# Optimization experiments

Measured on AMD Instinct MI355X. Metric: run time of the kernel, lower is better.

The kernel has to match this reference:

```python
import jax, jax.numpy as jnp
import numpy as np

B, T, S, D, F = 4, 2048, 2048, 256, 1024
EPS = 1e-5


def setup_inputs() -> dict:
    key = jax.random.key(0)
    ks = jax.random.split(key, 24)
    def lin(kw, kb, din, dout):
        w = jax.random.normal(kw, (din, dout), jnp.float32) / np.sqrt(din)
        b = jax.random.normal(kb, (dout,), jnp.float32) * 0.01
        return w, b
    Wq1, bq1 = lin(ks[0], ks[1], D, D)
    Wk1, bk1 = lin(ks[2], ks[3], D, D)
    Wv1, bv1 = lin(ks[4], ks[5], D, D)
    Wq2, bq2 = lin(ks[6], ks[7], D, D)
    Wk2, bk2 = lin(ks[8], ks[9], D, D)
    Wv2, bv2 = lin(ks[10], ks[11], D, D)
    W1, b1 = lin(ks[12], ks[13], D, F)
    W2, b2 = lin(ks[14], ks[15], F, D)
    y = jax.random.normal(ks[16], (B, T, D), jnp.float32)
    Z = jax.random.normal(ks[17], (B, S, D), jnp.float32)
    target_mask = jnp.tril(jnp.ones((T, T), jnp.int32))  # causal 0/1 mask
    return dict(y=y, Z=Z, target_mask=target_mask,
                Wq1=Wq1, bq1=bq1, Wk1=Wk1, bk1=bk1, Wv1=Wv1, bv1=bv1,
                Wq2=Wq2, bq2=bq2, Wk2=Wk2, bk2=bk2, Wv2=Wv2, bv2=bv2,
                W1=W1, b1=b1, W2=W2, b2=b2,
                g1=jnp.ones((D,), jnp.float32), be1=jnp.zeros((D,), jnp.float32),
                g2=jnp.ones((D,), jnp.float32), be2=jnp.zeros((D,), jnp.float32),
                g3=jnp.ones((D,), jnp.float32), be3=jnp.zeros((D,), jnp.float32))


def _ln(x, g, b):
    m = x.mean(-1, keepdims=True)
    v = ((x - m) ** 2).mean(-1, keepdims=True)
    return (x - m) / jnp.sqrt(v + EPS) * g + b


def _attn(Q, K, V, mask=None):
    scale = 1.0 / np.sqrt(Q.shape[-1]).astype(np.float32)
    scores = jnp.einsum('btd,bsd->bts', Q, K) * scale  # [B,T,S]
    if mask is not None:
        scores = jnp.where(mask == 0, -jnp.inf, scores)
    probs = jax.nn.softmax(scores, axis=-1)
    return jnp.einsum('bts,bsd->btd', probs, V)


def reference(y, Z, target_mask, Wq1, bq1, Wk1, bk1, Wv1, bv1,
              Wq2, bq2, Wk2, bk2, Wv2, bv2, W1, b1, W2, b2,
              g1, be1, g2, be2, g3, be3):
    # self attention
    sa = _attn(y @ Wq1 + bq1, y @ Wk1 + bk1, y @ Wv1 + bv1, target_mask)
    y1 = _ln(y + sa, g1, be1)
    # cross attention
    ca = _attn(y1 @ Wq2 + bq2, Z @ Wk2 + bk2, Z @ Wv2 + bv2)
    y2 = _ln(y1 + ca, g2, be2)
    # FFN
    ffn = jax.nn.relu(y2 @ W1 + b1) @ W2 + b2
    return _ln(y2 + ffn, g3, be3)
```

## Files before the change

kernel.cpp:

```cpp
#include <hip/hip_runtime.h>

#define B_ 4
#define T_ 2048
#define S_ 2048
#define D_ 256
#define F_ 1024

typedef unsigned short ushort_t;
typedef __bf16 v8bf __attribute__((ext_vector_type(8)));
typedef float v4f __attribute__((ext_vector_type(4)));
typedef __attribute__((address_space(1))) const unsigned int gas_uint;
typedef __attribute__((address_space(3))) unsigned int las_uint;

__device__ __forceinline__ ushort_t f2bf(float f) {
  unsigned u = __float_as_uint(f);
  unsigned r = (u + 0x7FFFu + ((u >> 16) & 1u)) >> 16;
  return (ushort_t)r;
}

struct WP { const float* s; ushort_t* d; int K, N; };
struct WP8 { WP m[8]; };

__global__ void prep_weights_k(WP8 a) {
  WP w = a.m[blockIdx.z];
  int k0 = blockIdx.x * 64, n0 = blockIdx.y * 64;
  if (k0 >= w.K || n0 >= w.N) return;
  __shared__ ushort_t tile[64][65];
  int tx = threadIdx.x, ty = threadIdx.y;
  for (int r = ty; r < 64; r += 4)
    tile[r][tx] = f2bf(w.s[(size_t)(k0 + r) * w.N + n0 + tx]);
  __syncthreads();
  for (int r = ty; r < 64; r += 4)
    w.d[(size_t)(n0 + r) * w.K + k0 + tx] = tile[tx][r];
}

__global__ void cvt_k(const float* __restrict__ a, ushort_t* __restrict__ oa,
                      const float* __restrict__ b, ushort_t* __restrict__ ob) {
  int i = blockIdx.x * 256 + threadIdx.x;
  const float* s = blockIdx.y ? b : a;
  ushort_t* d = blockIdx.y ? ob : oa;
  size_t off = (size_t)i * 8;
  float4 v0 = *(const float4*)(s + off);
  float4 v1 = *(const float4*)(s + off + 4);
  union { ushort_t u[8]; uint4 v; } pk;
  pk.u[0] = f2bf(v0.x); pk.u[1] = f2bf(v0.y); pk.u[2] = f2bf(v0.z); pk.u[3] = f2bf(v0.w);
  pk.u[4] = f2bf(v1.x); pk.u[5] = f2bf(v1.y); pk.u[6] = f2bf(v1.z); pk.u[7] = f2bf(v1.w);
  *(uint4*)(d + off) = pk.v;
}

__global__ void transpose_bf16_k(const ushort_t* __restrict__ in, ushort_t* __restrict__ out,
                                 int rows, int cols) {
  in  += (size_t)blockIdx.z * rows * cols;
  out += (size_t)blockIdx.z * rows * cols;
  __shared__ ushort_t tile[64][65];
  int r0 = blockIdx.x * 64, c0 = blockIdx.y * 64;
  int tx = threadIdx.x, ty = threadIdx.y;
  for (int r = ty; r < 64; r += 4)
    tile[r][tx] = in[(size_t)(r0 + r) * cols + c0 + tx];
  __syncthreads();
  for (int r = ty; r < 64; r += 4)
    out[(size_t)(c0 + r) * rows + r0 + tx] = tile[tx][r];
}

template<bool RELU>
__global__ __launch_bounds__(256, 2) void gemm_bt(
    const ushort_t* __restrict__ A, int lda, long long sAz,
    const ushort_t* __restrict__ Bt, int ldb, long long sBz,
    const float* __restrict__ bias,
    float* __restrict__ Cf, ushort_t* __restrict__ Cb, int ldc, long long sCz,
    int K, float alpha, int causal, int crow0) {
  const int n0 = blockIdx.x * 64, m0 = blockIdx.y * 128;
  if (causal && n0 > crow0 + m0 + 127) return;
  A  += (long long)blockIdx.z * sAz;
  Bt += (long long)blockIdx.z * sBz;
  const long long coff = (long long)blockIdx.z * sCz;
  const int t = threadIdx.x, lane = t & 63, wv = t >> 6;
  const int wm = wv >> 1, wn = wv & 1;
  const int kslot = lane >> 4, l15 = lane & 15;
  __shared__ __align__(16) char smem[24576];
  char* sA = smem;
  char* sB = smem + 16384;

  v4f acc[4][2];
  v4f zero = {0.f, 0.f, 0.f, 0.f};
#pragma unroll
  for (int m = 0; m < 4; ++m)
#pragma unroll
    for (int n = 0; n < 2; ++n) acc[m][n] = zero;

  for (int kk = 0; kk < K; kk += 64) {
    __syncthreads();
#pragma unroll
    for (int q = 0; q < 4; ++q) {
      int g = q * 256 + t;
      int row = g >> 3, j = g & 7;
      const ushort_t* src = A + (long long)(m0 + row) * lda + kk + ((j ^ (row & 7)) << 3);
      __builtin_amdgcn_global_load_lds((gas_uint*)src,
          (las_uint*)(sA + q * 4096 + (wv << 10)), 16, 0, 0);
    }
#pragma unroll
    for (int q = 0; q < 2; ++q) {
      int g = q * 256 + t;
      int row = g >> 3, j = g & 7;
      const ushort_t* src = Bt + (long long)(n0 + row) * ldb + kk + ((j ^ (row & 7)) << 3);
      __builtin_amdgcn_global_load_lds((gas_uint*)src,
          (las_uint*)(sB + q * 4096 + (wv << 10)), 16, 0, 0);
    }
    __syncthreads();
#pragma unroll
    for (int ks = 0; ks < 2; ++ks) {
      v8bf af[4]; v8bf bfr[2];
#pragma unroll
      for (int m = 0; m < 4; ++m) {
        int row = wm * 64 + m * 16 + l15;
        int gs = (ks * 4 + kslot) ^ (row & 7);
        af[m] = *(const v8bf*)(sA + ((row * 8 + gs) << 4));
      }
#pragma unroll
      for (int n = 0; n < 2; ++n) {
        int row = wn * 32 + n * 16 + l15;
        int gs = (ks * 4 + kslot) ^ (row & 7);
        bfr[n] = *(const v8bf*)(sB + ((row * 8 + gs) << 4));
      }
#pragma unroll
      for (int m = 0; m < 4; ++m)
#pragma unroll
        for (int n = 0; n < 2; ++n)
          acc[m][n] = __builtin_amdgcn_mfma_f32_16x16x32_bf16(af[m], bfr[n], acc[m][n], 0, 0, 0);
    }
  }
#pragma unroll
  for (int m = 0; m < 4; ++m) {
    int grow0 = m0 + wm * 64 + m * 16 + (kslot << 2);
#pragma unroll
    for (int n = 0; n < 2; ++n) {
      int gcol = n0 + wn * 32 + n * 16 + l15;
      float bb = bias ? bias[gcol] : 0.f;
#pragma unroll
      for (int i = 0; i < 4; ++i) {
        float v = acc[m][n][i] * alpha + bb;
        if (RELU) v = fmaxf(v, 0.f);
        long long off = coff + (long long)(grow0 + i) * ldc + gcol;
        if (Cf) Cf[off] = v;
        if (Cb) Cb[off] = f2bf(v);
      }
    }
  }
}

__global__ __launch_bounds__(256) void softmax_k(float* scores, int causal, int crow0) {
  int row = blockIdx.x;
  float* rp = scores + ((size_t)blockIdx.y * T_ + row) * S_;
  int t = threadIdx.x;
  int valid = causal ? crow0 + row + 1 : S_;
  float x[8];
  float4 v0 = *(const float4*)(rp + t * 8);
  float4 v1 = *(const float4*)(rp + t * 8 + 4);
  x[0] = v0.x; x[1] = v0.y; x[2] = v0.z; x[3] = v0.w;
  x[4] = v1.x; x[5] = v1.y; x[6] = v1.z; x[7] = v1.w;
  float m = -3.0e38f;
#pragma unroll
  for (int j = 0; j < 8; ++j) if (t * 8 + j < valid) m = fmaxf(m, x[j]);
  for (int mk = 1; mk < 64; mk <<= 1) m = fmaxf(m, __shfl_xor(m, mk));
  __shared__ float rbuf[8];
  if ((t & 63) == 0) rbuf[t >> 6] = m;
  __syncthreads();
  m = fmaxf(fmaxf(rbuf[0], rbuf[1]), fmaxf(rbuf[2], rbuf[3]));
  float p[8]; float l = 0.f;
#pragma unroll
  for (int j = 0; j < 8; ++j) { p[j] = (t * 8 + j < valid) ? __expf(x[j] - m) : 0.f; l += p[j]; }
  for (int mk = 1; mk < 64; mk <<= 1) l += __shfl_xor(l, mk);
  if ((t & 63) == 0) rbuf[4 + (t >> 6)] = l;
  __syncthreads();
  l = rbuf[4] + rbuf[5] + rbuf[6] + rbuf[7];
  float inv = 1.f / l;
  union { ushort_t u[8]; uint4 v; } pk;
#pragma unroll
  for (int j = 0; j < 8; ++j) pk.u[j] = f2bf(p[j] * inv);
  __syncthreads();
  *(uint4*)((ushort_t*)rp + t * 8) = pk.v;
}

__global__ __launch_bounds__(256) void add_ln_k(
    const float* __restrict__ base, const float* __restrict__ delta,
    const float* __restrict__ g, const float* __restrict__ be,
    float* __restrict__ outf, ushort_t* __restrict__ outb) {
  int row = blockIdx.x * 4 + (threadIdx.x >> 6);
  int lane = threadIdx.x & 63;
  size_t off = (size_t)row * 256 + lane * 4;
  float4 xv = *(const float4*)(base + off);
  float4 dv = *(const float4*)(delta + off);
  float s0 = xv.x + dv.x, s1 = xv.y + dv.y, s2 = xv.z + dv.z, s3 = xv.w + dv.w;
  float sum = s0 + s1 + s2 + s3;
  for (int mk = 1; mk < 64; mk <<= 1) sum += __shfl_xor(sum, mk);
  float mean = sum * (1.f / 256.f);
  float e0 = s0 - mean, e1 = s1 - mean, e2 = s2 - mean, e3 = s3 - mean;
  float ss = e0 * e0 + e1 * e1 + e2 * e2 + e3 * e3;
  for (int mk = 1; mk < 64; mk <<= 1) ss += __shfl_xor(ss, mk);
  float rstd = rsqrtf(ss * (1.f / 256.f) + 1e-5f);
  float4 gv = *(const float4*)(g + lane * 4);
  float4 bv = *(const float4*)(be + lane * 4);
  float o0 = e0 * rstd * gv.x + bv.x, o1 = e1 * rstd * gv.y + bv.y;
  float o2 = e2 * rstd * gv.z + bv.z, o3 = e3 * rstd * gv.w + bv.w;
  float4 ov; ov.x = o0; ov.y = o1; ov.z = o2; ov.w = o3;
  *(float4*)(outf + off) = ov;
  if (outb) {
    union { ushort_t u[4]; uint2 v; } pk;
    pk.u[0] = f2bf(o0); pk.u[1] = f2bf(o1); pk.u[2] = f2bf(o2); pk.u[3] = f2bf(o3);
    *(uint2*)(outb + off) = pk.v;
  }
}

extern "C" void kernel_launch(void* const* d_in, const int* in_sizes, int n_in,
                              void* d_out, int out_size, void* d_ws, size_t ws_size,
                              hipStream_t stream) {
  const float* y   = (const float*)d_in[0];
  const float* Z   = (const float*)d_in[1];
  const float* Wq1 = (const float*)d_in[3];  const float* bq1 = (const float*)d_in[4];
  const float* Wk1 = (const float*)d_in[5];  const float* bk1 = (const float*)d_in[6];
  const float* Wv1 = (const float*)d_in[7];  const float* bv1 = (const float*)d_in[8];
  const float* Wq2 = (const float*)d_in[9];  const float* bq2 = (const float*)d_in[10];
  const float* Wk2 = (const float*)d_in[11]; const float* bk2 = (const float*)d_in[12];
  const float* Wv2 = (const float*)d_in[13]; const float* bv2 = (const float*)d_in[14];
  const float* W1  = (const float*)d_in[15]; const float* b1  = (const float*)d_in[16];
  const float* W2  = (const float*)d_in[17]; const float* b2  = (const float*)d_in[18];
  const float* g1  = (const float*)d_in[19]; const float* be1 = (const float*)d_in[20];
  const float* g2  = (const float*)d_in[21]; const float* be2 = (const float*)d_in[22];
  const float* g3  = (const float*)d_in[23]; const float* be3 = (const float*)d_in[24];
  float* out = (float*)d_out;

  char* p = (char*)d_ws;
  auto alloc = [&](size_t sz) { char* r = p; p += (sz + 255) & ~(size_t)255; return r; };
  const size_t NBT = (size_t)B_ * T_ * D_;
  ushort_t* Wq1t = (ushort_t*)alloc(D_ * D_ * 2);
  ushort_t* Wk1t = (ushort_t*)alloc(D_ * D_ * 2);
  ushort_t* Wv1t = (ushort_t*)alloc(D_ * D_ * 2);
  ushort_t* Wq2t = (ushort_t*)alloc(D_ * D_ * 2);
  ushort_t* Wk2t = (ushort_t*)alloc(D_ * D_ * 2);
  ushort_t* Wv2t = (ushort_t*)alloc(D_ * D_ * 2);
  ushort_t* W1t  = (ushort_t*)alloc((size_t)F_ * D_ * 2);
  ushort_t* W2t  = (ushort_t*)alloc((size_t)D_ * F_ * 2);
  ushort_t* yb  = (ushort_t*)alloc(NBT * 2);
  ushort_t* Zb  = (ushort_t*)alloc(NBT * 2);
  float*    y1f = (float*)alloc(NBT * 4);
  ushort_t* y1b = (ushort_t*)alloc(NBT * 2);
  float*    y2f = (float*)alloc(NBT * 4);
  ushort_t* y2b = (ushort_t*)alloc(NBT * 2);
  ushort_t* Qb = (ushort_t*)alloc(NBT * 2);
  ushort_t* Kb = (ushort_t*)alloc(NBT * 2);
  ushort_t* Vb = (ushort_t*)alloc(NBT * 2);
  ushort_t* Vt = (ushort_t*)alloc(NBT * 2);
  ushort_t* Hb = Qb;
  float* tmp = (float*)alloc(NBT * 4);
  float* scores = (float*)p;
  size_t remain = (ws_size > (size_t)(p - (char*)d_ws))
                      ? ws_size - (size_t)(p - (char*)d_ws) : 0;
  const size_t rowb = (size_t)S_ * 4;
  int CH = 0, TC = 0;
  if (remain >= (size_t)B_ * T_ * rowb)      { CH = B_; TC = T_; }
  else if (remain >= (size_t)T_ * rowb)      { CH = 1;  TC = T_; }
  else {
    int tc = (int)(remain / (rowb * 128)) * 128;
    if (tc > T_) tc = T_;
    CH = 1; TC = tc;
  }

  WP8 wp;
  wp.m[0] = {Wq1, Wq1t, D_, D_}; wp.m[1] = {Wk1, Wk1t, D_, D_};
  wp.m[2] = {Wv1, Wv1t, D_, D_}; wp.m[3] = {Wq2, Wq2t, D_, D_};
  wp.m[4] = {Wk2, Wk2t, D_, D_}; wp.m[5] = {Wv2, Wv2t, D_, D_};
  wp.m[6] = {W1, W1t, D_, F_};   wp.m[7] = {W2, W2t, F_, D_};
  prep_weights_k<<<dim3(16, 16, 8), dim3(64, 4), 0, stream>>>(wp);
  cvt_k<<<dim3((int)(NBT / 8 / 256), 2), 256, 0, stream>>>(y, yb, Z, Zb);

  auto gemm = [&](const ushort_t* A, int lda, long long sAz,
                  const ushort_t* Bt, int ldb, long long sBz,
                  const float* bias, float* Cf, ushort_t* Cb, int ldc, long long sCz,
                  int M, int N, int K, float alpha, int causal, bool relu, int Zn, int crow0) {
    dim3 g(N / 64, M / 128, Zn);
    if (relu)
      gemm_bt<true><<<g, 256, 0, stream>>>(A, lda, sAz, Bt, ldb, sBz, bias, Cf, Cb, ldc, sCz, K, alpha, causal, crow0);
    else
      gemm_bt<false><<<g, 256, 0, stream>>>(A, lda, sAz, Bt, ldb, sBz, bias, Cf, Cb, ldc, sCz, K, alpha, causal, crow0);
  };

  auto attention = [&](const ushort_t* Q, const ushort_t* Kc, const ushort_t* Vc,
                       float* attout, int causal) {
    transpose_bf16_k<<<dim3(S_ / 64, D_ / 64, B_), dim3(64, 4), 0, stream>>>(Vc, Vt, S_, D_);
    if (TC <= 0) return;
    for (int b0 = 0; b0 < B_; b0 += CH) {
      for (int t0 = 0; t0 < T_; t0 += TC) {
        int rows = (t0 + TC <= T_) ? TC : (T_ - t0);
        gemm(Q + ((size_t)b0 * T_ + t0) * D_, D_, (long long)T_ * D_,
             Kc + (size_t)b0 * S_ * D_, D_, (long long)S_ * D_,
             nullptr, scores, nullptr, S_, (long long)T_ * S_,
             rows, S_, D_, 0.0625f, causal, false, CH, t0);
        softmax_k<<<dim3(rows, CH), 256, 0, stream>>>(scores, causal, t0);
        gemm((const ushort_t*)scores, 2 * S_, (long long)T_ * 2 * S_,
             Vt + (size_t)b0 * D_ * S_, S_, (long long)D_ * S_,
             nullptr, attout + ((size_t)b0 * T_ + t0) * D_, nullptr, D_, (long long)T_ * D_,
             rows, D_, S_, 1.f, 0, false, CH, 0);
      }
    }
  };

  gemm(yb, D_, 0, Wq1t, D_, 0, bq1, nullptr, Qb, D_, 0, B_ * T_, D_, D_, 1.f, 0, false, 1, 0);
  gemm(yb, D_, 0, Wk1t, D_, 0, bk1, nullptr, Kb, D_, 0, B_ * T_, D_, D_, 1.f, 0, false, 1, 0);
  gemm(yb, D_, 0, Wv1t, D_, 0, bv1, nullptr, Vb, D_, 0, B_ * T_, D_, D_, 1.f, 0, false, 1, 0);
  attention(Qb, Kb, Vb, tmp, 1);
  add_ln_k<<<dim3(B_ * T_ / 4), 256, 0, stream>>>(y, tmp, g1, be1, y1f, y1b);

  gemm(y1b, D_, 0, Wq2t, D_, 0, bq2, nullptr, Qb, D_, 0, B_ * T_, D_, D_, 1.f, 0, false, 1, 0);
  gemm(Zb,  D_, 0, Wk2t, D_, 0, bk2, nullptr, Kb, D_, 0, B_ * S_, D_, D_, 1.f, 0, false, 1, 0);
  gemm(Zb,  D_, 0, Wv2t, D_, 0, bv2, nullptr, Vb, D_, 0, B_ * S_, D_, D_, 1.f, 0, false, 1, 0);
  attention(Qb, Kb, Vb, tmp, 0);
  add_ln_k<<<dim3(B_ * T_ / 4), 256, 0, stream>>>(y1f, tmp, g2, be2, y2f, y2b);

  gemm(y2b, D_, 0, W1t, D_, 0, b1, nullptr, Hb, F_, 0, B_ * T_, F_, D_, 1.f, 0, true, 1, 0);
  gemm(Hb, F_, 0, W2t, F_, 0, b2, tmp, nullptr, D_, 0, B_ * T_, D_, F_, 1.f, 0, false, 1, 0);
  add_ln_k<<<dim3(B_ * T_ / 4), 256, 0, stream>>>(y2f, tmp, g3, be3, out, nullptr);
}
```

Baseline: 364.5 us.

## Fuse QKV projections, store scores in bf16, and skip masked K-tiles in PV

Merges the Q/K/V projection GEMMs into one wide GEMM writing an interleaved QKV buffer with packed biases, and merges the cross-attention K/V projections the same way. Attention scores are now written directly as bf16 instead of fp32, so softmax and the probability-by-value GEMM move half the bytes. The probability-by-value GEMM also stops its K loop at the causal diagonal. This relies on the transposed weight buffers being laid out contiguously so one GEMM covers Wq/Wk/Wv, and pre-softmax scores lose precision when rounded to bf16.

```diff
diff --git a/kernel.cpp b/kernel.cpp
--- a/kernel.cpp
+++ b/kernel.cpp
@@ -16,6 +16,9 @@
   unsigned u = __float_as_uint(f);
   unsigned r = (u + 0x7FFFu + ((u >> 16) & 1u)) >> 16;
   return (ushort_t)r;
+}
+__device__ __forceinline__ float bf2f(ushort_t u) {
+  return __uint_as_float((unsigned)u << 16);
 }
 
 struct WP { const float* s; ushort_t* d; int K, N; };
@@ -32,6 +35,14 @@
   __syncthreads();
   for (int r = ty; r < 64; r += 4)
     w.d[(size_t)(n0 + r) * w.K + k0 + tx] = tile[tx][r];
+}
+
+__global__ void pack_bias_k(const float* bq1, const float* bk1, const float* bv1,
+                            const float* bk2, const float* bv2,
+                            float* bqkv1, float* bkv2) {
+  int t = blockIdx.x * 256 + threadIdx.x;
+  if (t < 768) bqkv1[t] = (t < 256) ? bq1[t] : (t < 512) ? bk1[t - 256] : bv1[t - 512];
+  if (t < 512) bkv2[t] = (t < 256) ? bk2[t] : bv2[t - 256];
 }
 
 __global__ void cvt_k(const float* __restrict__ a, ushort_t* __restrict__ oa,
@@ -48,15 +59,16 @@
   *(uint4*)(d + off) = pk.v;
 }
 
-__global__ void transpose_bf16_k(const ushort_t* __restrict__ in, ushort_t* __restrict__ out,
+__global__ void transpose_bf16_k(const ushort_t* __restrict__ in, long long sIz, int ldin,
+                                 ushort_t* __restrict__ out, long long sOz,
                                  int rows, int cols) {
-  in  += (size_t)blockIdx.z * rows * cols;
-  out += (size_t)blockIdx.z * rows * cols;
+  in  += (size_t)blockIdx.z * sIz;
+  out += (size_t)blockIdx.z * sOz;
   __shared__ ushort_t tile[64][65];
   int r0 = blockIdx.x * 64, c0 = blockIdx.y * 64;
   int tx = threadIdx.x, ty = threadIdx.y;
   for (int r = ty; r < 64; r += 4)
-    tile[r][tx] = in[(size_t)(r0 + r) * cols + c0 + tx];
+    tile[r][tx] = in[(size_t)(r0 + r) * ldin + c0 + tx];
   __syncthreads();
   for (int r = ty; r < 64; r += 4)
     out[(size_t)(c0 + r) * rows + r0 + tx] = tile[tx][r];
@@ -68,9 +80,10 @@
     const ushort_t* __restrict__ Bt, int ldb, long long sBz,
     const float* __restrict__ bias,
     float* __restrict__ Cf, ushort_t* __restrict__ Cb, int ldc, long long sCz,
-    int K, float alpha, int causal, int crow0) {
+    int K, float alpha, int causal, int kcausal, int crow0) {
   const int n0 = blockIdx.x * 64, m0 = blockIdx.y * 128;
   if (causal && n0 > crow0 + m0 + 127) return;
+  const int Keff = kcausal ? ((crow0 + m0 + 128 < K) ? crow0 + m0 + 128 : K) : K;
   A  += (long long)blockIdx.z * sAz;
   Bt += (long long)blockIdx.z * sBz;
   const long long coff = (long long)blockIdx.z * sCz;
@@ -88,7 +101,7 @@
 #pragma unroll
     for (int n = 0; n < 2; ++n) acc[m][n] = zero;
 
-  for (int kk = 0; kk < K; kk += 64) {
+  for (int kk = 0; kk < Keff; kk += 64) {
     __syncthreads();
 #pragma unroll
     for (int q = 0; q < 4; ++q) {
@@ -148,16 +161,16 @@
   }
 }
 
-__global__ __launch_bounds__(256) void softmax_k(float* scores, int causal, int crow0) {
+__global__ __launch_bounds__(256) void softmax_k(ushort_t* sc, int causal, int crow0) {
   int row = blockIdx.x;
-  float* rp = scores + ((size_t)blockIdx.y * T_ + row) * S_;
+  ushort_t* rp = sc + ((size_t)blockIdx.y * T_ + row) * S_;
   int t = threadIdx.x;
   int valid = causal ? crow0 + row + 1 : S_;
+  union { ushort_t u[8]; uint4 v; } in;
+  in.v = *(const uint4*)(rp + t * 8);
   float x[8];
-  float4 v0 = *(const float4*)(rp + t * 8);
-  float4 v1 = *(const float4*)(rp + t * 8 + 4);
-  x[0] = v0.x; x[1] = v0.y; x[2] = v0.z; x[3] = v0.w;
-  x[4] = v1.x; x[5] = v1.y; x[6] = v1.z; x[7] = v1.w;
+#pragma unroll
+  for (int j = 0; j < 8; ++j) x[j] = bf2f(in.u[j]);
   float m = -3.0e38f;
 #pragma unroll
   for (int j = 0; j < 8; ++j) if (t * 8 + j < valid) m = fmaxf(m, x[j]);
@@ -177,8 +190,7 @@
   union { ushort_t u[8]; uint4 v; } pk;
 #pragma unroll
   for (int j = 0; j < 8; ++j) pk.u[j] = f2bf(p[j] * inv);
-  __syncthreads();
-  *(uint4*)((ushort_t*)rp + t * 8) = pk.v;
+  *(uint4*)(rp + t * 8) = pk.v;
 }
 
 __global__ __launch_bounds__(256) void add_ln_k(
@@ -240,22 +252,22 @@
   ushort_t* Wv2t = (ushort_t*)alloc(D_ * D_ * 2);
   ushort_t* W1t  = (ushort_t*)alloc((size_t)F_ * D_ * 2);
   ushort_t* W2t  = (ushort_t*)alloc((size_t)D_ * F_ * 2);
+  float* bqkv1 = (float*)alloc(768 * 4);
+  float* bkv2  = (float*)alloc(512 * 4);
   ushort_t* yb  = (ushort_t*)alloc(NBT * 2);
   ushort_t* Zb  = (ushort_t*)alloc(NBT * 2);
   float*    y1f = (float*)alloc(NBT * 4);
   ushort_t* y1b = (ushort_t*)alloc(NBT * 2);
   float*    y2f = (float*)alloc(NBT * 4);
   ushort_t* y2b = (ushort_t*)alloc(NBT * 2);
-  ushort_t* Qb = (ushort_t*)alloc(NBT * 2);
-  ushort_t* Kb = (ushort_t*)alloc(NBT * 2);
-  ushort_t* Vb = (ushort_t*)alloc(NBT * 2);
-  ushort_t* Vt = (ushort_t*)alloc(NBT * 2);
-  ushort_t* Hb = Qb;
+  ushort_t* QKVb = (ushort_t*)alloc((size_t)B_ * T_ * 768 * 2);
+  ushort_t* Vt   = (ushort_t*)alloc(NBT * 2);
+  ushort_t* Hb = QKVb;
   float* tmp = (float*)alloc(NBT * 4);
-  float* scores = (float*)p;
+  ushort_t* sc = (ushort_t*)p;
   size_t remain = (ws_size > (size_t)(p - (char*)d_ws))
                       ? ws_size - (size_t)(p - (char*)d_ws) : 0;
-  const size_t rowb = (size_t)S_ * 4;
+  const size_t rowb = (size_t)S_ * 2;
   int CH = 0, TC = 0;
   if (remain >= (size_t)B_ * T_ * rowb)      { CH = B_; TC = T_; }
   else if (remain >= (size_t)T_ * rowb)      { CH = 1;  TC = T_; }
@@ -271,52 +283,58 @@
   wp.m[4] = {Wk2, Wk2t, D_, D_}; wp.m[5] = {Wv2, Wv2t, D_, D_};
   wp.m[6] = {W1, W1t, D_, F_};   wp.m[7] = {W2, W2t, F_, D_};
   prep_weights_k<<<dim3(16, 16, 8), dim3(64, 4), 0, stream>>>(wp);
+  pack_bias_k<<<dim3(5), 256, 0, stream>>>(bq1, bk1, bv1, bk2, bv2, bqkv1, bkv2);
   cvt_k<<<dim3((int)(NBT / 8 / 256), 2), 256, 0, stream>>>(y, yb, Z, Zb);
 
   auto gemm = [&](const ushort_t* A, int lda, long long sAz,
                   const ushort_t* Bt, int ldb, long long sBz,
                   const float* bias, float* Cf, ushort_t* Cb, int ldc, long long sCz,
-                  int M, int N, int K, float alpha, int causal, bool relu, int Zn, int crow0) {
+                  int M, int N, int K, float alpha, int causal, int kcausal,
+                  bool relu, int Zn, int crow0) {
     dim3 g(N / 64, M / 128, Zn);
     if (relu)
-      gemm_bt<true><<<g, 256, 0, stream>>>(A, lda, sAz, Bt, ldb, sBz, bias, Cf, Cb, ldc, sCz, K, alpha, causal, crow0);
+      gemm_bt<true><<<g, 256, 0, stream>>>(A, lda, sAz, Bt, ldb, sBz, bias, Cf, Cb, ldc, sCz, K, alpha, causal, kcausal, crow0);
     else
-      gemm_bt<false><<<g, 256, 0, stream>>>(A, lda, sAz, Bt, ldb, sBz, bias, Cf, Cb, ldc, sCz, K, alpha, causal, crow0);
+      gemm_bt<false><<<g, 256, 0, stream>>>(A, lda, sAz, Bt, ldb, sBz, bias, Cf, Cb, ldc, sCz, K, alpha, causal, kcausal, crow0);
   };
 
-  auto attention = [&](const ushort_t* Q, const ushort_t* Kc, const ushort_t* Vc,
-                       float* attout, int causal) {
-    transpose_bf16_k<<<dim3(S_ / 64, D_ / 64, B_), dim3(64, 4), 0, stream>>>(Vc, Vt, S_, D_);
+  auto attention = [&](float* attout, int causal) {
+    transpose_bf16_k<<<dim3(S_ / 64, D_ / 64, B_), dim3(64, 4), 0, stream>>>(
+        QKVb + 512, (long long)S_ * 768, 768, Vt, (long long)D_ * S_, S_, D_);
     if (TC <= 0) return;
+    const ushort_t* Q = QKVb;
+    const ushort_t* Kc = QKVb + 256;
     for (int b0 = 0; b0 < B_; b0 += CH) {
       for (int t0 = 0; t0 < T_; t0 += TC) {
         int rows = (t0 + TC <= T_) ? TC : (T_ - t0);
-        gemm(Q + ((size_t)b0 * T_ + t0) * D_, D_, (long long)T_ * D_,
-             Kc + (size_t)b0 * S_ * D_, D_, (long long)S_ * D_,
-             nullptr, scores, nullptr, S_, (long long)T_ * S_,
-             rows, S_, D_, 0.0625f, causal, false, CH, t0);
-        softmax_k<<<dim3(rows, CH), 256, 0, stream>>>(scores, causal, t0);
-        gemm((const ushort_t*)scores, 2 * S_, (long long)T_ * 2 * S_,
+        gemm(Q + ((size_t)b0 * T_ + t0) * 768, 768, (long long)T_ * 768,
+             Kc + (size_t)b0 * S_ * 768, 768, (long long)S_ * 768,
+             nullptr, nullptr, sc, S_, (long long)T_ * S_,
+             rows, S_, D_, 0.0625f, causal, 0, false, CH, t0);
+        softmax_k<<<dim3(rows, CH), 256, 0, stream>>>(sc, causal, t0);
+        gemm(sc, S_, (long long)T_ * S_,
              Vt + (size_t)b0 * D_ * S_, S_, (long long)D_ * S_,
              nullptr, attout + ((size_t)b0 * T_ + t0) * D_, nullptr, D_, (long long)T_ * D_,
-             rows, D_, S_, 1.f, 0, false, CH, 0);
+             rows, D_, S_, 1.f, 0, causal, false, CH, t0);
       }
     }
   };
 
-  gemm(yb, D_, 0, Wq1t, D_, 0, bq1, nullptr, Qb, D_, 0, B_ * T_, D_, D_, 1.f, 0, false, 1, 0);
-  gemm(yb, D_, 0, Wk1t, D_, 0, bk1, nullptr, Kb, D_, 0, B_ * T_, D_, D_, 1.f, 0, false, 1, 0);
-  gemm(yb, D_, 0, Wv1t, D_, 0, bv1, nullptr, Vb, D_, 0, B_ * T_, D_, D_, 1.f, 0, false, 1, 0);
-  attention(Qb, Kb, Vb, tmp, 1);
+  gemm(yb, D_, 0, Wq1t, D_, 0, bqkv1, nullptr, QKVb, 768, 0,
+       B_ * T_, 768, D_, 1.f, 0, 0, false, 1, 0);
+  attention(tmp, 1);
   add_ln_k<<<dim3(B_ * T_ / 4), 256, 0, stream>>>(y, tmp, g1, be1, y1f, y1b);
 
-  gemm(y1b, D_, 0, Wq2t, D_, 0, bq2, nullptr, Qb, D_, 0, B_ * T_, D_, D_, 1.f, 0, false, 1, 0);
-  gemm(Zb,  D_, 0, Wk2t, D_, 0, bk2, nullptr, Kb, D_, 0, B_ * S_, D_, D_, 1.f, 0, false, 1, 0);
-  gemm(Zb,  D_, 0, Wv2t, D_, 0, bv2, nullptr, Vb, D_, 0, B_ * S_, D_, D_, 1.f, 0, false, 1, 0);
-  attention(Qb, Kb, Vb, tmp, 0);
+  gemm(y1b, D_, 0, Wq2t, D_, 0, bq2, nullptr, QKVb, 768, 0,
+       B_ * T_, D_, D_, 1.f, 0, 0, false, 1, 0);
+  gemm(Zb, D_, 0, Wk2t, D_, 0, bkv2, nullptr, QKVb + 256, 768, 0,
+       B_ * S_, 512, D_, 1.f, 0, 0, false, 1, 0);
+  attention(tmp, 0);
   add_ln_k<<<dim3(B_ * T_ / 4), 256, 0, stream>>>(y1f, tmp, g2, be2, y2f, y2b);
 
-  gemm(y2b, D_, 0, W1t, D_, 0, b1, nullptr, Hb, F_, 0, B_ * T_, F_, D_, 1.f, 0, true, 1, 0);
-  gemm(Hb, F_, 0, W2t, F_, 0, b2, tmp, nullptr, D_, 0, B_ * T_, D_, F_, 1.f, 0, false, 1, 0);
+  gemm(y2b, D_, 0, W1t, D_, 0, b1, nullptr, Hb, F_, 0,
+       B_ * T_, F_, D_, 1.f, 0, 0, true, 1, 0);
+  gemm(Hb, F_, 0, W2t, F_, 0, b2, tmp, nullptr, D_, 0,
+       B_ * T_, D_, F_, 1.f, 0, 0, false, 1, 0);
   add_ln_k<<<dim3(B_ * T_ / 4), 256, 0, stream>>>(y2f, tmp, g3, be3, out, nullptr);
 }
```

New measurement: 336.4 us. 7.7% less time.
